# Kernel optimization log

Hardware: AMD Instinct MI355X
Metric: run time of the kernel (lower is better)

The kernel has to match this reference:

```python
import jax, jax.numpy as jnp
import numpy as np
from functools import partial

N_NODES = 20000
N_EDGES = 640000
IN_C = 64
HID = 256
OUT_C = 64
HIST = 12
HORIZON = 6


def gcn_conv(x, w, b, src, dst, deg_inv, norm):
    # PyG GCNConv with self loops: out = D^-1/2 (A+I) D^-1/2 (x @ w) + b
    xw = x @ w                                   # [N, H]
    agg = jax.ops.segment_sum(xw[src] * norm[:, None], dst, num_segments=N_NODES)
    return agg + xw * deg_inv[:, None] + b


def gru_cell(x, h, wih, whh, bih, bhh):
    # torch.nn.GRUCell semantics; wih: [3H, in], whh: [3H, H]
    gi = x @ wih.T + bih
    gh = h @ whh.T + bhh
    ir, iz, inn = jnp.split(gi, 3, axis=-1)
    hr, hz, hn = jnp.split(gh, 3, axis=-1)
    r = jax.nn.sigmoid(ir + hr)
    z = jax.nn.sigmoid(iz + hz)
    n = jnp.tanh(inn + r * hn)
    return (1.0 - z) * n + z * h


def setup_inputs() -> dict:
    key = jax.random.key(0)
    ks = jax.random.split(key, 20)
    s = lambda fan: 1.0 / np.sqrt(fan)
    inp = {
        "x_seq": jax.random.normal(ks[0], (1, HIST, N_NODES, IN_C), dtype=jnp.float32),
        "src": jax.random.randint(ks[1], (N_EDGES,), 0, N_NODES),
        "dst": jax.random.randint(ks[2], (N_EDGES,), 0, N_NODES),
        "gcn1_w": jax.random.normal(ks[3], (IN_C, HID), jnp.float32) * s(IN_C),
        "gcn1_b": jnp.zeros((HID,), jnp.float32),
        "gcn2_w": jax.random.normal(ks[4], (HID, HID), jnp.float32) * s(HID),
        "gcn2_b": jnp.zeros((HID,), jnp.float32),
        "proj_w": jax.random.normal(ks[5], (HID, OUT_C), jnp.float32) * s(HID),
        "proj_b": jnp.zeros((OUT_C,), jnp.float32),
    }
    for i, name in enumerate(["gru1", "gru2", "gru3"]):
        k1, k2 = jax.random.split(ks[6 + i])
        inp[f"{name}_wih"] = jax.random.normal(k1, (3 * HID, HID), jnp.float32) * s(HID)
        inp[f"{name}_whh"] = jax.random.normal(k2, (3 * HID, HID), jnp.float32) * s(HID)
        inp[f"{name}_bih"] = jnp.zeros((3 * HID,), jnp.float32)
        inp[f"{name}_bhh"] = jnp.zeros((3 * HID,), jnp.float32)
    return inp


def reference(x_seq, src, dst, gcn1_w, gcn1_b, gcn2_w, gcn2_b, proj_w, proj_b,
              gru1_wih, gru1_whh, gru1_bih, gru1_bhh,
              gru2_wih, gru2_whh, gru2_bih, gru2_bhh,
              gru3_wih, gru3_whh, gru3_bih, gru3_bhh):
    # symmetric GCN normalization with self loops (static graph -> compute once)
    deg = jax.ops.segment_sum(jnp.ones((N_EDGES,), jnp.float32), dst, num_segments=N_NODES) + 1.0
    deg_is = deg ** -0.5
    norm = deg_is[src] * deg_is[dst]   # per-edge norm
    deg_inv = 1.0 / deg                # self-loop norm

    def cell(xt, h1, h2, h3):
        x = jax.nn.relu(gcn_conv(xt, gcn1_w, gcn1_b, src, dst, deg_inv, norm))
        x = jax.nn.relu(gcn_conv(x, gcn2_w, gcn2_b, src, dst, deg_inv, norm))
        h1 = gru_cell(x, h1, gru1_wih, gru1_whh, gru1_bih, gru1_bhh)
        h2 = gru_cell(h1, h2, gru2_wih, gru2_whh, gru2_bih, gru2_bhh)
        h3 = gru_cell(h2, h3, gru3_wih, gru3_whh, gru3_bih, gru3_bhh)
        return h1, h2, h3

    h0 = jnp.zeros((N_NODES, HID), jnp.float32)

    def enc_step(carry, xt):
        return cell(xt, *carry), None

    (h1, h2, h3), _ = jax.lax.scan(enc_step, (h0, h0, h0), x_seq[0])  # [T,N,C]

    def dec_step(carry, _):
        h1, h2, h3, xd = carry
        h1, h2, h3 = cell(xd, h1, h2, h3)
        y = h3 @ proj_w + proj_b       # [N, OUT_C]
        return (h1, h2, h3, y), y

    _, ys = jax.lax.scan(dec_step, (h1, h2, h3, x_seq[0, -1]), None, length=HORIZON)
    return ys[None]  # [1, HORIZON, N, OUT_C]
```

## Files before the change

### kernel.cpp

```cpp
#include <hip/hip_runtime.h>

#define N_NODESC 20000
#define N_EDGESC 640000

typedef _Float16 f16;
typedef __attribute__((ext_vector_type(4))) _Float16 f16x4;
typedef __attribute__((ext_vector_type(8))) _Float16 f16x8;
typedef __attribute__((ext_vector_type(4))) float f32x4;

__device__ __forceinline__ f32x4 mfma16(f16x8 a, f16x8 b, f32x4 c){
  return __builtin_amdgcn_mfma_f32_16x16x32_f16(a, b, c, 0, 0, 0);
}
__device__ __forceinline__ float sigm(float x){ return 1.f/(1.f+__expf(-x)); }
__device__ __forceinline__ float tanh_(float x){
  x = fminf(fmaxf(x, -15.f), 15.f);
  float e = __expf(-2.f*x);
  return (1.f - e)/(1.f + e);
}
__device__ __forceinline__ void stage16(const void* g, void* l){
  __builtin_amdgcn_global_load_lds((const __attribute__((address_space(1))) unsigned int*)g,
                                   (__attribute__((address_space(3))) unsigned int*)l, 16, 0, 0);
}
#define SB       __builtin_amdgcn_sched_barrier(0)
#define AS_VM(n) do{ asm volatile("s_waitcnt vmcnt(" #n ")" ::: "memory"); SB; }while(0)
#define BAR      do{ __builtin_amdgcn_s_barrier(); SB; }while(0)

__global__ __launch_bounds__(256) void k_hist(const int* __restrict__ dst, int* __restrict__ cnt){
  int e = blockIdx.x*256 + threadIdx.x;
  if(e < N_EDGESC) atomicAdd(&cnt[dst[e]], 1);
}

__global__ __launch_bounds__(256) void k_scanA(const int* __restrict__ cnt,
    int* __restrict__ row_ptr, int* __restrict__ btot){
  __shared__ int ws[4];
  int b = blockIdx.x, t = threadIdx.x;
  int i = b*256 + t;
  int v = (i < N_NODESC) ? cnt[i] : 0;
  int lane = t&63, wv = t>>6;
  int incl = v;
  #pragma unroll
  for(int off=1; off<64; off<<=1){ int u = __shfl_up(incl, off); if(lane>=off) incl += u; }
  if(lane==63) ws[wv] = incl;
  __syncthreads();
  int woff = 0;
  for(int k=0;k<wv;k++) woff += ws[k];
  if(i < N_NODESC) row_ptr[i] = woff + incl - v;
  if(t == 255) btot[b] = woff + incl;
}

__global__ __launch_bounds__(128) void k_scanB(const int* __restrict__ btot,
    int* __restrict__ boff, int* __restrict__ row_ptr){
  __shared__ int s[128];
  int t = threadIdx.x;
  int orig = (t < 79) ? btot[t] : 0;
  s[t] = orig;
  __syncthreads();
  #pragma unroll
  for(int off=1; off<128; off<<=1){
    int u = (t>=off) ? s[t-off] : 0;
    __syncthreads();
    s[t] += u;
    __syncthreads();
  }
  if(t < 79) boff[t] = s[t] - orig;
  if(t == 0) row_ptr[N_NODESC] = N_EDGESC;
}

__global__ __launch_bounds__(256) void k_scanC(const int* __restrict__ cnt,
    const int* __restrict__ boff, int* __restrict__ row_ptr,
    float* __restrict__ deg_inv, float* __restrict__ deg_is){
  int i = blockIdx.x*256 + threadIdx.x;
  if(i >= N_NODESC) return;
  row_ptr[i] += boff[blockIdx.x];
  float d = (float)(cnt[i] + 1);
  deg_inv[i] = 1.f/d;
  deg_is[i]  = rsqrtf(d);
}

__global__ __launch_bounds__(256) void k_fill(const int* __restrict__ src, const int* __restrict__ dst,
    const int* __restrict__ row_ptr, int* __restrict__ cursor, const float* __restrict__ deg_is,
    int2* __restrict__ ev){
  int e = blockIdx.x*256 + threadIdx.x;
  if(e >= N_EDGESC) return;
  int d = dst[e], s = src[e];
  int p = atomicAdd(&cursor[d], 1);
  int2 v;
  v.x = s;
  v.y = __float_as_int(deg_is[s]*deg_is[d]);
  ev[row_ptr[d] + p] = v;
}

__global__ __launch_bounds__(256) void k_cvt(const float* __restrict__ x, f16* __restrict__ o, int n4){
  int i = blockIdx.x*256 + threadIdx.x;
  if(i >= n4) return;
  f32x4 v = *(const f32x4*)(x + (size_t)i*4);
  *(f16x4*)(o + (size_t)i*4) = __builtin_convertvector(v, f16x4);
}

__global__ __launch_bounds__(256) void k_pack(const float* __restrict__ w, f16* __restrict__ dstp,
    int K, int NO, int trans){
  int t = blockIdx.x*256 + threadIdx.x;
  if(t >= K*NO) return;
  int i = t&7, g = (t>>3)&3, rest = t>>5;
  int c = rest % NO, kb = rest / NO;
  int k = kb*32 + g*8 + i;
  float v = trans ? w[(size_t)c*K + k] : w[(size_t)k*NO + c];
  dstp[t] = (f16)v;
}

__global__ __launch_bounds__(256) void k_agg64(const f16* __restrict__ x,
    const int* __restrict__ row_ptr, const int2* __restrict__ ev,
    const float* __restrict__ deg_inv, f16* __restrict__ O){
  int n = (blockIdx.x*256 + threadIdx.x)>>6;
  int c = threadIdx.x&63;
  if(n >= N_NODESC) return;
  float acc = deg_inv[n]*(float)x[(size_t)n*64 + c];
  int e0 = row_ptr[n], e1 = row_ptr[n+1];
  int e = e0;
  for(; e+4<=e1; e+=4){
    int2 a=ev[e], b=ev[e+1], cc=ev[e+2], d=ev[e+3];
    float v0=(float)x[(size_t)a.x*64+c],  v1=(float)x[(size_t)b.x*64+c];
    float v2=(float)x[(size_t)cc.x*64+c], v3=(float)x[(size_t)d.x*64+c];
    acc += __int_as_float(a.y)*v0 + __int_as_float(b.y)*v1
         + __int_as_float(cc.y)*v2 + __int_as_float(d.y)*v3;
  }
  for(; e<e1; e++){ int2 a=ev[e]; acc += __int_as_float(a.y)*(float)x[(size_t)a.x*64+c]; }
  O[(size_t)n*64+c] = (f16)acc;
}

__global__ __launch_bounds__(256) void k_agg256(const f16* __restrict__ x1,
    const int* __restrict__ row_ptr, const int2* __restrict__ ev,
    const float* __restrict__ deg_inv, f16* __restrict__ O){
  int n = (blockIdx.x*256 + threadIdx.x)>>6;
  int lane = threadIdx.x&63;
  if(n >= N_NODESC) return;
  const f16x4* xv = (const f16x4*)x1;
  f32x4 acc = __builtin_convertvector(xv[(size_t)n*64 + lane], f32x4) * deg_inv[n];
  int e0 = row_ptr[n], e1 = row_ptr[n+1];
  int e = e0;
  for(; e+4<=e1; e+=4){
    int2 a=ev[e], b=ev[e+1], cc=ev[e+2], d=ev[e+3];
    f32x4 v0=__builtin_convertvector(xv[(size_t)a.x*64+lane],  f32x4);
    f32x4 v1=__builtin_convertvector(xv[(size_t)b.x*64+lane],  f32x4);
    f32x4 v2=__builtin_convertvector(xv[(size_t)cc.x*64+lane], f32x4);
    f32x4 v3=__builtin_convertvector(xv[(size_t)d.x*64+lane],  f32x4);
    acc += v0*__int_as_float(a.y); acc += v1*__int_as_float(b.y);
    acc += v2*__int_as_float(cc.y); acc += v3*__int_as_float(d.y);
  }
  for(; e<e1; e++){ int2 a=ev[e];
    acc += __builtin_convertvector(xv[(size_t)a.x*64+lane], f32x4)*__int_as_float(a.y); }
  ((f16x4*)O)[(size_t)n*64+lane] = __builtin_convertvector(acc, f16x4);
}

__global__ __launch_bounds__(256) void k_gcn1(const f16* __restrict__ A,
    const f16* __restrict__ Bp, const float* __restrict__ bias, f16* __restrict__ C){
  __shared__ f16x8 ldsv[512];
  char* lds = (char*)ldsv;
  const int tid = threadIdx.x, lane = tid&63, w = tid>>6, l15 = lane&15, q = lane>>4;
  const int m0 = blockIdx.x*64;
  int rg = m0 + lane; if(rg > N_NODESC-1) rg = N_NODESC-1;
  #pragma unroll
  for(int i=0;i<2;i++){
    int region = i*4 + w;
    int kbb = region>>2, qq = region&3;
    stage16((const char*)A + (size_t)rg*128 + kbb*64 + qq*16, lds + region*1024 + lane*16);
  }
  AS_VM(0);
  BAR;
  f32x4 acc[4][4];
  #pragma unroll
  for(int rt=0;rt<4;rt++)
    #pragma unroll
    for(int ct=0;ct<4;ct++) acc[rt][ct] = (f32x4){0.f,0.f,0.f,0.f};
  #pragma unroll
  for(int kb=0;kb<2;kb++){
    f16x8 bf[4];
    #pragma unroll
    for(int ct=0;ct<4;ct++){
      int c = w*64 + ct*16 + l15;
      bf[ct] = *(const f16x8*)(Bp + ((unsigned)(kb*256 + c)*4 + q)*8);
    }
    #pragma unroll
    for(int rt=0;rt<4;rt++){
      f16x8 ah = *(const f16x8*)(lds + (kb*4+q)*1024 + (rt*16+l15)*16);
      #pragma unroll
      for(int ct=0;ct<4;ct++)
        acc[rt][ct] = mfma16(ah, bf[ct], acc[rt][ct]);
    }
  }
  #pragma unroll
  for(int rt=0;rt<4;rt++)
    #pragma unroll
    for(int ct=0;ct<4;ct++){
      int c = w*64 + ct*16 + l15;
      float bv = bias[c];
      #pragma unroll
      for(int j=0;j<4;j++){
        int r = m0 + rt*16 + q*4 + j;
        if(r < N_NODESC) C[(size_t)r*256 + c] = (f16)fmaxf(acc[rt][ct][j] + bv, 0.f);
      }
    }
}

__global__ __launch_bounds__(256,3) void k_gcn2(const f16* __restrict__ A,
    const f16* __restrict__ Bp, const float* __restrict__ bias, f16* __restrict__ C){
  __shared__ f16x8 ldsv[2048];
  char* lds = (char*)ldsv;
  const int tid = threadIdx.x, lane = tid&63, w = tid>>6, l15 = lane&15, q = lane>>4;
  const int m0 = blockIdx.x*64;
  int rg = m0 + lane; if(rg > N_NODESC-1) rg = N_NODESC-1;
  const size_t abyte = (size_t)rg*512;
  #pragma unroll
  for(int kb=0;kb<8;kb++)
    stage16((const char*)A + abyte + kb*64 + w*16, lds + kb*4096 + w*1024 + lane*16);
  f32x4 acc[4][4];
  #pragma unroll
  for(int rt=0;rt<4;rt++)
    #pragma unroll
    for(int ct=0;ct<4;ct++) acc[rt][ct] = (f32x4){0.f,0.f,0.f,0.f};
  f16x8 bf[3][4];
  const int cbase = w*64 + l15;
  #pragma unroll
  for(int s=0;s<2;s++)
    #pragma unroll
    for(int ct=0;ct<4;ct++)
      bf[s][ct] = *(const f16x8*)(Bp + ((unsigned)(s*256 + cbase + ct*16)*4 + q)*8);
  AS_VM(0);
  BAR;
  #pragma unroll
  for(int kb=0;kb<8;kb++){
    const int s = kb%3;
    if(kb<6){
      const int ns = (kb+2)%3;
      #pragma unroll
      for(int ct=0;ct<4;ct++)
        bf[ns][ct] = *(const f16x8*)(Bp + ((unsigned)((kb+2)*256 + cbase + ct*16)*4 + q)*8);
    }
    __builtin_amdgcn_s_setprio(1);
    #pragma unroll
    for(int rt=0;rt<4;rt++){
      f16x8 ah = *(const f16x8*)(lds + kb*4096 + q*1024 + (rt*16+l15)*16);
      #pragma unroll
      for(int ct=0;ct<4;ct++)
        acc[rt][ct] = mfma16(ah, bf[s][ct], acc[rt][ct]);
    }
    __builtin_amdgcn_s_setprio(0);
  }
  #pragma unroll
  for(int rt=0;rt<4;rt++)
    #pragma unroll
    for(int ct=0;ct<4;ct++){
      int c = cbase + ct*16;
      float bv = bias[c];
      #pragma unroll
      for(int j=0;j<4;j++){
        int r = m0 + rt*16 + q*4 + j;
        if(r < N_NODESC) C[(size_t)r*256 + c] = (f16)fmaxf(acc[rt][ct][j] + bv, 0.f);
      }
    }
}

__global__ __launch_bounds__(256,2) void k_gru(
    const f16* __restrict__ X, const f16* __restrict__ H, f16* __restrict__ Nh,
    const f16* __restrict__ Wi, const f16* __restrict__ Wh,
    const float* __restrict__ bih, const float* __restrict__ bhh){
  __shared__ f16x8 ldsv[4096];
  char* lds = (char*)ldsv;
  const int NB = 1252, QQ = NB>>3, RR = NB&7;
  int bid = blockIdx.x;
  int xcd = bid & 7, jj = bid >> 3;
  int nid = (xcd < RR) ? xcd*(QQ+1) + jj : RR*(QQ+1) + (xcd-RR)*QQ + jj;
  const int m0 = (nid>>2)*64;
  const int cb = nid&3;
  const int tid = threadIdx.x, lane = tid&63, w = tid>>6, l15 = lane&15, q = lane>>4;
  const int cc = cb*64 + w*16 + l15;
  int rg = m0 + lane; if(rg > N_NODESC-1) rg = N_NODESC-1;
  const size_t abyte = (size_t)rg*512;
  const f16* pl[2] = {X, H};
  #pragma unroll
  for(int p=0;p<2;p++)
    #pragma unroll
    for(int kb=0;kb<8;kb++)
      stage16((const char*)pl[p] + abyte + kb*64 + w*16,
              lds + p*32768 + kb*4096 + w*1024 + lane*16);
  f32x4 acc[6][4];
  #pragma unroll
  for(int m=0;m<6;m++)
    #pragma unroll
    for(int rt=0;rt<4;rt++) acc[m][rt] = (f32x4){0.f,0.f,0.f,0.f};
  const unsigned wbase = (unsigned)cc*32 + q*8;
  f16x8 bi[3][3], bh[3][3];
  #pragma unroll
  for(int s=0;s<2;s++){
    unsigned wo = wbase + (unsigned)s*24576u;
    bi[s][0] = *(const f16x8*)(Wi + wo);
    bi[s][1] = *(const f16x8*)(Wi + wo + 8192);
    bi[s][2] = *(const f16x8*)(Wi + wo + 16384);
    bh[s][0] = *(const f16x8*)(Wh + wo);
    bh[s][1] = *(const f16x8*)(Wh + wo + 8192);
    bh[s][2] = *(const f16x8*)(Wh + wo + 16384);
  }
  AS_VM(0);
  BAR;
  #pragma unroll
  for(int kb=0;kb<8;kb++){
    const int s = kb%3;
    if(kb<6){
      const int ns = (kb+2)%3;
      unsigned wo = wbase + (unsigned)(kb+2)*24576u;
      bi[ns][0] = *(const f16x8*)(Wi + wo);
      bi[ns][1] = *(const f16x8*)(Wi + wo + 8192);
      bi[ns][2] = *(const f16x8*)(Wi + wo + 16384);
      bh[ns][0] = *(const f16x8*)(Wh + wo);
      bh[ns][1] = *(const f16x8*)(Wh + wo + 8192);
      bh[ns][2] = *(const f16x8*)(Wh + wo + 16384);
    }
    __builtin_amdgcn_s_setprio(1);
    #pragma unroll
    for(int rt=0;rt<4;rt++){
      const int ro = kb*4096 + q*1024 + (rt*16+l15)*16;
      f16x8 ax = *(const f16x8*)(lds + ro);
      f16x8 ah = *(const f16x8*)(lds + 32768 + ro);
      acc[0][rt] = mfma16(ax, bi[s][0], acc[0][rt]);
      acc[1][rt] = mfma16(ax, bi[s][1], acc[1][rt]);
      acc[2][rt] = mfma16(ax, bi[s][2], acc[2][rt]);
      acc[3][rt] = mfma16(ah, bh[s][0], acc[3][rt]);
      acc[4][rt] = mfma16(ah, bh[s][1], acc[4][rt]);
      acc[5][rt] = mfma16(ah, bh[s][2], acc[5][rt]);
    }
    __builtin_amdgcn_s_setprio(0);
  }
  float bir=bih[cc], biz=bih[cc+256], bin=bih[cc+512];
  float bhr=bhh[cc], bhz=bhh[cc+256], bhn=bhh[cc+512];
  #pragma unroll
  for(int rt=0;rt<4;rt++){
    #pragma unroll
    for(int j=0;j<4;j++){
      int r = m0 + rt*16 + q*4 + j;
      if(r < N_NODESC){
        float ir=acc[0][rt][j], iz=acc[1][rt][j], in_=acc[2][rt][j];
        float hr=acc[3][rt][j], hz=acc[4][rt][j], hn=acc[5][rt][j];
        float rgt = sigm(ir+bir + hr+bhr);
        float zg = sigm(iz+biz + hz+bhz);
        float ng = tanh_(in_+bin + rgt*(hn+bhn));
        float ho = (float)H[(size_t)r*256 + cc];
        float v = (1.f-zg)*ng + zg*ho;
        Nh[(size_t)r*256 + cc] = (f16)v;
      }
    }
  }
}

__global__ __launch_bounds__(256,4) void k_proj(const f16* __restrict__ A,
    const f16* __restrict__ Bp, const float* __restrict__ bias,
    float* __restrict__ C, f16* __restrict__ Cf16){
  __shared__ f16x8 ldsv[2048];
  char* lds = (char*)ldsv;
  const int tid = threadIdx.x, lane = tid&63, w = tid>>6, l15 = lane&15, q = lane>>4;
  const int m0 = blockIdx.x*64;
  const int cc = w*16 + l15;
  int rg = m0 + lane; if(rg > N_NODESC-1) rg = N_NODESC-1;
  const size_t abyte = (size_t)rg*512;
  #pragma unroll
  for(int kb=0;kb<8;kb++)
    stage16((const char*)A + abyte + kb*64 + w*16, lds + kb*4096 + w*1024 + lane*16);
  f32x4 acc[4];
  #pragma unroll
  for(int rt=0;rt<4;rt++) acc[rt] = (f32x4){0.f,0.f,0.f,0.f};
  f16x8 bf[3];
  bf[0] = *(const f16x8*)(Bp + ((unsigned)(0*64 + cc)*4 + q)*8);
  bf[1] = *(const f16x8*)(Bp + ((unsigned)(1*64 + cc)*4 + q)*8);
  AS_VM(0);
  BAR;
  #pragma unroll
  for(int kb=0;kb<8;kb++){
    const int s = kb%3;
    if(kb<6)
      bf[(kb+2)%3] = *(const f16x8*)(Bp + ((unsigned)((kb+2)*64 + cc)*4 + q)*8);
    #pragma unroll
    for(int rt=0;rt<4;rt++){
      f16x8 ah = *(const f16x8*)(lds + kb*4096 + q*1024 + (rt*16+l15)*16);
      acc[rt] = mfma16(ah, bf[s], acc[rt]);
    }
  }
  #pragma unroll
  for(int rt=0;rt<4;rt++){
    float bv = bias[cc];
    #pragma unroll
    for(int j=0;j<4;j++){
      int r = m0 + rt*16 + q*4 + j;
      if(r < N_NODESC){
        float v = acc[rt][j] + bv;
        C[(size_t)r*64 + cc] = v;
        Cf16[(size_t)r*64 + cc] = (f16)v;
      }
    }
  }
}

extern "C" void kernel_launch(void* const* d_in, const int* in_sizes, int n_in,
                              void* d_out, int out_size, void* d_ws, size_t ws_size,
                              hipStream_t stream){
  const float* x_seq  = (const float*)d_in[0];
  const int*   srcp   = (const int*)  d_in[1];
  const int*   dstp   = (const int*)  d_in[2];
  const float* gcn1_w = (const float*)d_in[3];
  const float* gcn1_b = (const float*)d_in[4];
  const float* gcn2_w = (const float*)d_in[5];
  const float* gcn2_b = (const float*)d_in[6];
  const float* proj_w = (const float*)d_in[7];
  const float* proj_b = (const float*)d_in[8];
  const float* wih[3] = {(const float*)d_in[9],  (const float*)d_in[13], (const float*)d_in[17]};
  const float* whh[3] = {(const float*)d_in[10], (const float*)d_in[14], (const float*)d_in[18]};
  const float* bih[3] = {(const float*)d_in[11], (const float*)d_in[15], (const float*)d_in[19]};
  const float* bhh[3] = {(const float*)d_in[12], (const float*)d_in[16], (const float*)d_in[20]};
  float* out = (float*)d_out;

  const size_t NP = (size_t)N_NODESC*256;
  char* p = (char*)d_ws;
  auto alloc = [&](size_t bytes)->char*{ char* r = p; p += (bytes + 255) & ~(size_t)255; return r; };
  int*   deg_cnt = (int*)  alloc((size_t)2*N_NODESC*4);
  int*   cursor  = deg_cnt + N_NODESC;
  int*   row_ptr = (int*)  alloc((size_t)(N_NODESC+1)*4);
  float* deg_inv = (float*)alloc((size_t)N_NODESC*4);
  float* deg_is  = (float*)alloc((size_t)N_NODESC*4);
  int*   btot    = (int*)  alloc((size_t)128*4);
  int*   boff    = (int*)  alloc((size_t)128*4);
  int2*  ev      = (int2*) alloc((size_t)N_EDGESC*8);
  f16* xf16 = (f16*)alloc((size_t)12*N_NODESC*64*2);
  f16* xdec = (f16*)alloc((size_t)N_NODESC*64*2);
  f16* z64  = (f16*)alloc((size_t)N_NODESC*64*2);
  f16* x1   = (f16*)alloc(NP*2);
  f16* xa   = (f16*)alloc(NP*2);
  f16* hbuf = (f16*)alloc((size_t)2*3*NP*2);
  f16* pk_gcn1 = (f16*)alloc((size_t)64*256*2);
  f16* pk_gcn2 = (f16*)alloc((size_t)256*256*2);
  f16* pk_proj = (f16*)alloc((size_t)256*64*2);
  f16* pk_wi[3]; f16* pk_wh[3];
  for(int i=0;i<3;i++){ pk_wi[i]=(f16*)alloc((size_t)256*768*2); pk_wh[i]=(f16*)alloc((size_t)256*768*2); }

  hipMemsetAsync(deg_cnt, 0, (size_t)2*N_NODESC*4, stream);
  hipMemsetAsync(hbuf,    0, (size_t)3*NP*2, stream);

  k_hist <<<2500,256,0,stream>>>(dstp, deg_cnt);
  k_scanA<<<79,  256,0,stream>>>(deg_cnt, row_ptr, btot);
  k_scanB<<<1,   128,0,stream>>>(btot, boff, row_ptr);
  k_scanC<<<79,  256,0,stream>>>(deg_cnt, boff, row_ptr, deg_inv, deg_is);
  k_fill <<<2500,256,0,stream>>>(srcp, dstp, row_ptr, cursor, deg_is, ev);
  k_cvt  <<<15000,256,0,stream>>>(x_seq, xf16, 12*N_NODESC*64/4);

  k_pack<<<64, 256,0,stream>>>(gcn1_w, pk_gcn1, 64, 256, 0);
  k_pack<<<256,256,0,stream>>>(gcn2_w, pk_gcn2, 256,256, 0);
  k_pack<<<64, 256,0,stream>>>(proj_w, pk_proj, 256, 64, 0);
  for(int i=0;i<3;i++){
    k_pack<<<768,256,0,stream>>>(wih[i], pk_wi[i], 256, 768, 1);
    k_pack<<<768,256,0,stream>>>(whh[i], pk_wh[i], 256, 768, 1);
  }

  auto Hs = [&](int slot, int g)->f16*{ return hbuf + ((size_t)(slot*3+g))*NP; };

  for(int s=0; s<18; s++){
    const f16* xt;
    if(s < 12)       xt = xf16 + (size_t)s*N_NODESC*64;
    else if(s == 12) xt = xf16 + (size_t)11*N_NODESC*64;
    else             xt = xdec;
    int cur = s&1, nxt = cur^1;

    k_agg64 <<<5000,256,0,stream>>>(xt, row_ptr, ev, deg_inv, z64);
    k_gcn1  <<<313, 256,0,stream>>>(z64, pk_gcn1, gcn1_b, x1);
    k_agg256<<<5000,256,0,stream>>>(x1, row_ptr, ev, deg_inv, xa);
    k_gcn2  <<<313, 256,0,stream>>>(xa, pk_gcn2, gcn2_b, xa);

    k_gru<<<1252,256,0,stream>>>(xa,        Hs(cur,0), Hs(nxt,0), pk_wi[0], pk_wh[0], bih[0], bhh[0]);
    k_gru<<<1252,256,0,stream>>>(Hs(nxt,0), Hs(cur,1), Hs(nxt,1), pk_wi[1], pk_wh[1], bih[1], bhh[1]);
    k_gru<<<1252,256,0,stream>>>(Hs(nxt,1), Hs(cur,2), Hs(nxt,2), pk_wi[2], pk_wh[2], bih[2], bhh[2]);

    if(s >= 12)
      k_proj<<<313,256,0,stream>>>(Hs(nxt,2), pk_proj, proj_b, out + (size_t)(s-12)*N_NODESC*64, xdec);
  }
}
```

Baseline: 3.686 ms.

## Stage GEMM A-tiles row-major with XOR swizzle and reuse staged H in GRU

```diff
diff --git a/kernel.cpp b/kernel.cpp
--- a/kernel.cpp
+++ b/kernel.cpp
@@ -152,18 +152,20 @@
   ((f16x4*)O)[(size_t)n*64+lane] = __builtin_convertvector(acc, f16x4);
 }
 
+
 __global__ __launch_bounds__(256) void k_gcn1(const f16* __restrict__ A,
     const f16* __restrict__ Bp, const float* __restrict__ bias, f16* __restrict__ C){
   __shared__ f16x8 ldsv[512];
   char* lds = (char*)ldsv;
   const int tid = threadIdx.x, lane = tid&63, w = tid>>6, l15 = lane&15, q = lane>>4;
   const int m0 = blockIdx.x*64;
-  int rg = m0 + lane; if(rg > N_NODESC-1) rg = N_NODESC-1;
   #pragma unroll
   for(int i=0;i<2;i++){
-    int region = i*4 + w;
-    int kbb = region>>2, qq = region&3;
-    stage16((const char*)A + (size_t)rg*128 + kbb*64 + qq*16, lds + region*1024 + lane*16);
+    const int o = i*4096 + tid*16;
+    const int row = o>>7, s = (o>>4)&7;
+    const int c = s ^ (row&7);
+    int rgs = m0 + row; if(rgs > N_NODESC-1) rgs = N_NODESC-1;
+    stage16((const char*)A + (size_t)rgs*128 + c*16, lds + o);
   }
   AS_VM(0);
   BAR;
@@ -172,6 +174,7 @@
   for(int rt=0;rt<4;rt++)
     #pragma unroll
     for(int ct=0;ct<4;ct++) acc[rt][ct] = (f32x4){0.f,0.f,0.f,0.f};
+  const int l7 = l15&7;
   #pragma unroll
   for(int kb=0;kb<2;kb++){
     f16x8 bf[4];
@@ -180,9 +183,10 @@
       int c = w*64 + ct*16 + l15;
       bf[ct] = *(const f16x8*)(Bp + ((unsigned)(kb*256 + c)*4 + q)*8);
     }
+    const int swz = ((kb*4+q) ^ l7)<<4;
     #pragma unroll
     for(int rt=0;rt<4;rt++){
-      f16x8 ah = *(const f16x8*)(lds + (kb*4+q)*1024 + (rt*16+l15)*16);
+      f16x8 ah = *(const f16x8*)(lds + (rt*16+l15)*128 + swz);
       #pragma unroll
       for(int ct=0;ct<4;ct++)
         acc[rt][ct] = mfma16(ah, bf[ct], acc[rt][ct]);
@@ -208,11 +212,14 @@
   char* lds = (char*)ldsv;
   const int tid = threadIdx.x, lane = tid&63, w = tid>>6, l15 = lane&15, q = lane>>4;
   const int m0 = blockIdx.x*64;
-  int rg = m0 + lane; if(rg > N_NODESC-1) rg = N_NODESC-1;
-  const size_t abyte = (size_t)rg*512;
-  #pragma unroll
-  for(int kb=0;kb<8;kb++)
-    stage16((const char*)A + abyte + kb*64 + w*16, lds + kb*4096 + w*1024 + lane*16);
+  #pragma unroll
+  for(int i=0;i<8;i++){
+    const int o = i*4096 + tid*16;
+    const int row = o>>9, s = (o>>4)&31;
+    const int c = s ^ (row&7);
+    int rgs = m0 + row; if(rgs > N_NODESC-1) rgs = N_NODESC-1;
+    stage16((const char*)A + (size_t)rgs*512 + c*16, lds + o);
+  }
   f32x4 acc[4][4];
   #pragma unroll
   for(int rt=0;rt<4;rt++)
@@ -227,6 +234,7 @@
       bf[s][ct] = *(const f16x8*)(Bp + ((unsigned)(s*256 + cbase + ct*16)*4 + q)*8);
   AS_VM(0);
   BAR;
+  const int l7 = l15&7;
   #pragma unroll
   for(int kb=0;kb<8;kb++){
     const int s = kb%3;
@@ -236,10 +244,11 @@
       for(int ct=0;ct<4;ct++)
         bf[ns][ct] = *(const f16x8*)(Bp + ((unsigned)((kb+2)*256 + cbase + ct*16)*4 + q)*8);
     }
+    const int swz = ((kb*4+q) ^ l7)<<4;
     __builtin_amdgcn_s_setprio(1);
     #pragma unroll
     for(int rt=0;rt<4;rt++){
-      f16x8 ah = *(const f16x8*)(lds + kb*4096 + q*1024 + (rt*16+l15)*16);
+      f16x8 ah = *(const f16x8*)(lds + (rt*16+l15)*512 + swz);
       #pragma unroll
       for(int ct=0;ct<4;ct++)
         acc[rt][ct] = mfma16(ah, bf[s][ct], acc[rt][ct]);
@@ -274,15 +283,17 @@
   const int cb = nid&3;
   const int tid = threadIdx.x, lane = tid&63, w = tid>>6, l15 = lane&15, q = lane>>4;
   const int cc = cb*64 + w*16 + l15;
-  int rg = m0 + lane; if(rg > N_NODESC-1) rg = N_NODESC-1;
-  const size_t abyte = (size_t)rg*512;
   const f16* pl[2] = {X, H};
   #pragma unroll
-  for(int p=0;p<2;p++)
-    #pragma unroll
-    for(int kb=0;kb<8;kb++)
-      stage16((const char*)pl[p] + abyte + kb*64 + w*16,
-              lds + p*32768 + kb*4096 + w*1024 + lane*16);
+  for(int i=0;i<16;i++){
+    const int o = i*4096 + tid*16;
+    const int p = o>>15;
+    const int rem = o & 32767;
+    const int row = rem>>9, s = (rem>>4)&31;
+    const int c = s ^ (row&7);
+    int rgs = m0 + row; if(rgs > N_NODESC-1) rgs = N_NODESC-1;
+    stage16((const char*)pl[p] + (size_t)rgs*512 + c*16, lds + o);
+  }
   f32x4 acc[6][4];
   #pragma unroll
   for(int m=0;m<6;m++)
@@ -302,6 +313,7 @@
   }
   AS_VM(0);
   BAR;
+  const int l7 = l15&7;
   #pragma unroll
   for(int kb=0;kb<8;kb++){
     const int s = kb%3;
@@ -315,10 +327,11 @@
       bh[ns][1] = *(const f16x8*)(Wh + wo + 8192);
       bh[ns][2] = *(const f16x8*)(Wh + wo + 16384);
     }
+    const int swz = ((kb*4+q) ^ l7)<<4;
     __builtin_amdgcn_s_setprio(1);
     #pragma unroll
     for(int rt=0;rt<4;rt++){
-      const int ro = kb*4096 + q*1024 + (rt*16+l15)*16;
+      const int ro = (rt*16+l15)*512 + swz;
       f16x8 ax = *(const f16x8*)(lds + ro);
       f16x8 ah = *(const f16x8*)(lds + 32768 + ro);
       acc[0][rt] = mfma16(ax, bi[s][0], acc[0][rt]);
@@ -332,20 +345,23 @@
   }
   float bir=bih[cc], biz=bih[cc+256], bin=bih[cc+512];
   float bhr=bhh[cc], bhz=bhh[cc+256], bhn=bhh[cc+512];
+  const int hcc = (cc>>3);
+  const int hlo = (cc&7)*2;
   #pragma unroll
   for(int rt=0;rt<4;rt++){
     #pragma unroll
     for(int j=0;j<4;j++){
-      int r = m0 + rt*16 + q*4 + j;
-      if(r < N_NODESC){
+      int r = rt*16 + q*4 + j;
+      int grow = m0 + r;
+      if(grow < N_NODESC){
         float ir=acc[0][rt][j], iz=acc[1][rt][j], in_=acc[2][rt][j];
         float hr=acc[3][rt][j], hz=acc[4][rt][j], hn=acc[5][rt][j];
         float rgt = sigm(ir+bir + hr+bhr);
         float zg = sigm(iz+biz + hz+bhz);
         float ng = tanh_(in_+bin + rgt*(hn+bhn));
-        float ho = (float)H[(size_t)r*256 + cc];
+        float ho = (float)*(const f16*)(lds + 32768 + r*512 + ((hcc ^ (r&7))<<4) + hlo);
         float v = (1.f-zg)*ng + zg*ho;
-        Nh[(size_t)r*256 + cc] = (f16)v;
+        Nh[(size_t)grow*256 + cc] = (f16)v;
       }
     }
   }
@@ -359,11 +375,14 @@
   const int tid = threadIdx.x, lane = tid&63, w = tid>>6, l15 = lane&15, q = lane>>4;
   const int m0 = blockIdx.x*64;
   const int cc = w*16 + l15;
-  int rg = m0 + lane; if(rg > N_NODESC-1) rg = N_NODESC-1;
-  const size_t abyte = (size_t)rg*512;
-  #pragma unroll
-  for(int kb=0;kb<8;kb++)
-    stage16((const char*)A + abyte + kb*64 + w*16, lds + kb*4096 + w*1024 + lane*16);
+  #pragma unroll
+  for(int i=0;i<8;i++){
+    const int o = i*4096 + tid*16;
+    const int row = o>>9, s = (o>>4)&31;
+    const int c = s ^ (row&7);
+    int rgs = m0 + row; if(rgs > N_NODESC-1) rgs = N_NODESC-1;
+    stage16((const char*)A + (size_t)rgs*512 + c*16, lds + o);
+  }
   f32x4 acc[4];
   #pragma unroll
   for(int rt=0;rt<4;rt++) acc[rt] = (f32x4){0.f,0.f,0.f,0.f};
@@ -372,14 +391,16 @@
   bf[1] = *(const f16x8*)(Bp + ((unsigned)(1*64 + cc)*4 + q)*8);
   AS_VM(0);
   BAR;
+  const int l7 = l15&7;
   #pragma unroll
   for(int kb=0;kb<8;kb++){
     const int s = kb%3;
     if(kb<6)
       bf[(kb+2)%3] = *(const f16x8*)(Bp + ((unsigned)((kb+2)*64 + cc)*4 + q)*8);
+    const int swz = ((kb*4+q) ^ l7)<<4;
     #pragma unroll
     for(int rt=0;rt<4;rt++){
-      f16x8 ah = *(const f16x8*)(lds + kb*4096 + q*1024 + (rt*16+l15)*16);
+      f16x8 ah = *(const f16x8*)(lds + (rt*16+l15)*512 + swz);
       acc[rt] = mfma16(ah, bf[s], acc[rt]);
     }
   }
```

After: 3.424 ms. 7.1% less time.
